# Kernel tuning notes

Hardware: AMD Instinct MI355X
Metric: run time of the kernel (lower is better)

## Reference

```python
import jax, jax.numpy as jnp
import numpy as np
from jax import lax

DIM = 256
STATE = 64
D_INNER = 256          # ssd_expand=1 * dim
HIDDEN = 4 * DIM       # mlp_ratio=4
CONV_DIM = 3 * STATE
B, H, W = 16, 64, 64
EPS = 1e-5


def dwconv(x, w, b=None):
    # depthwise 3x3, SAME padding; x:(B,C,H,W) w:(C,1,3,3)
    y = lax.conv_general_dilated(x, w, (1, 1), 'SAME',
                                 feature_group_count=x.shape[1],
                                 dimension_numbers=('NCHW', 'OIHW', 'NCHW'))
    if b is not None:
        y = y + b[None, :, None, None]
    return y


def batchnorm(x, g, b):
    m = x.mean(axis=(0, 2, 3), keepdims=True)
    v = x.var(axis=(0, 2, 3), keepdims=True)
    return (x - m) * jax.lax.rsqrt(v + EPS) * g[None, :, None, None] + b[None, :, None, None]


def layernorm1d(x, w, b):
    # norm over channel dim of (B,C,L)
    m = x.mean(axis=1, keepdims=True)
    v = x.var(axis=1, keepdims=True)
    return (x - m) * jax.lax.rsqrt(v + EPS) * w[None, :, None] + b[None, :, None]


def pw1d(x, w, b):
    # 1x1 conv1d: x:(B,Cin,L), w:(Cout,Cin)
    return jnp.einsum('oc,bcl->bol', w, x) + b[None, :, None]


def setup_inputs() -> dict:
    key = jax.random.key(0)
    ks = jax.random.split(key, 16)
    s = 0.02
    inp = {
        'x': jax.random.normal(ks[0], (B, DIM, H, W), jnp.float32),
        'alpha': 1e-4 * jnp.ones((4, DIM), jnp.float32),
        'dw1_w': s * jax.random.normal(ks[1], (DIM, 1, 3, 3), jnp.float32),
        'bn1_g': jnp.ones((DIM,), jnp.float32),
        'bn1_b': jnp.zeros((DIM,), jnp.float32),
        'dw2_w': s * jax.random.normal(ks[2], (DIM, 1, 3, 3), jnp.float32),
        'bn2_g': jnp.ones((DIM,), jnp.float32),
        'bn2_b': jnp.zeros((DIM,), jnp.float32),
        'ln_w': jnp.ones((DIM,), jnp.float32),
        'ln_b': jnp.zeros((DIM,), jnp.float32),
        'bcdt_w': s * jax.random.normal(ks[3], (CONV_DIM, DIM), jnp.float32),
        'bcdt_b': jnp.zeros((CONV_DIM,), jnp.float32),
        'mdw_w': s * jax.random.normal(ks[4], (CONV_DIM, 1, 3, 3), jnp.float32),
        'mdw_b': jnp.zeros((CONV_DIM,), jnp.float32),
        'hz_w': s * jax.random.normal(ks[5], (2 * D_INNER, DIM), jnp.float32),
        'hz_b': jnp.zeros((2 * D_INNER,), jnp.float32),
        'out_w': s * jax.random.normal(ks[6], (DIM, D_INNER), jnp.float32),
        'out_b': jnp.zeros((DIM,), jnp.float32),
        'A': jax.random.uniform(ks[7], (STATE,), jnp.float32, 1.0, 16.0),
        'D': jnp.ones((1,), jnp.float32),
        'ffn_w1': s * jax.random.normal(ks[8], (HIDDEN, DIM), jnp.float32),
        'ffn_b1': jnp.zeros((HIDDEN,), jnp.float32),
        'ffn_w2': s * jax.random.normal(ks[9], (DIM, HIDDEN), jnp.float32),
        'ffn_b2': jnp.zeros((DIM,), jnp.float32),
    }
    return inp


def _mixer(xf, bcdt_w, bcdt_b, mdw_w, mdw_b, hz_w, hz_b, out_w, out_b, A, D, h_, w_):
    # xf: (B, dim, L)
    b = xf.shape[0]
    BCdt = pw1d(xf, bcdt_w, bcdt_b).reshape(b, CONV_DIM, h_, w_)
    BCdt = dwconv(BCdt, mdw_w, mdw_b).reshape(b, CONV_DIM, h_ * w_)
    Bm, Cm, dt = jnp.split(BCdt, [STATE, 2 * STATE], axis=1)  # (B,S,L) each
    Am = jax.nn.softmax(dt + A[None, :, None], axis=-1)
    AB = Am * Bm                                   # (B,S,L)
    h = jnp.einsum('bcl,bsl->bcs', xf, AB)         # (B,dim,S) small
    hz = jnp.einsum('oc,bcs->bos', hz_w, h) + hz_b[None, :, None]
    hh, z = jnp.split(hz, [D_INNER], axis=1)
    hh = hh * jax.nn.silu(z) + hh * D[0]
    hh = jnp.einsum('oc,bcs->bos', out_w, hh) + out_b[None, :, None]
    y = jnp.einsum('bcs,bsl->bcl', hh, Cm)         # (B,dim,L)
    return y.reshape(b, DIM, h_, w_)


def reference(x, alpha, dw1_w, bn1_g, bn1_b, dw2_w, bn2_g, bn2_b, ln_w, ln_b,
              bcdt_w, bcdt_b, mdw_w, mdw_b, hz_w, hz_b, out_w, out_b, A, D,
              ffn_w1, ffn_b1, ffn_w2, ffn_b2):
    a = jax.nn.sigmoid(alpha)[:, None, :, None, None]  # (4,1,dim,1,1)
    x = (1 - a[0]) * x + a[0] * batchnorm(dwconv(x, dw1_w), bn1_g, bn1_b)
    x_prev = x
    b, _, h_, w_ = x.shape
    xf = layernorm1d(x.reshape(b, DIM, h_ * w_), ln_w, ln_b)
    y = _mixer(xf, bcdt_w, bcdt_b, mdw_w, mdw_b, hz_w, hz_b, out_w, out_b, A, D, h_, w_)
    x = (1 - a[1]) * x_prev + a[1] * y
    x = (1 - a[2]) * x + a[2] * batchnorm(dwconv(x, dw2_w), bn2_g, bn2_b)
    # FFN: 1x1 conv -> GELU -> 1x1 conv
    hdn = jax.nn.gelu(jnp.einsum('oc,bchw->bohw', ffn_w1, x) + ffn_b1[None, :, None, None])
    x_ffn = jnp.einsum('oc,bchw->bohw', ffn_w2, hdn) + ffn_b2[None, :, None, None]
    x = (1 - a[3]) * x + a[3] * x_ffn
    return x
```

## Files before the change

### kernel.cpp

```cpp
#include <hip/hip_runtime.h>
#include <stdint.h>


typedef __attribute__((ext_vector_type(8))) short bf16x8;
typedef __attribute__((ext_vector_type(4))) float f32x4;

__device__ __forceinline__ unsigned short f2b(float f){
  union { float f; unsigned int u; } v; v.f = f;
  unsigned int r = v.u + 0x7FFFu + ((v.u >> 16) & 1u);
  return (unsigned short)(r >> 16);
}
__device__ __forceinline__ float b2f(unsigned short h){
  union { unsigned int u; float f; } v; v.u = ((unsigned int)h) << 16;
  return v.f;
}
__device__ __forceinline__ float sigm(float x){ return 1.0f / (1.0f + __expf(-x)); }
__device__ __forceinline__ float gelu_fast(float v){
  float t = v * (-2.3022059f - 0.10294886f * v * v);
  float e = __builtin_amdgcn_exp2f(t);
  return v * __builtin_amdgcn_rcpf(1.0f + e);
}
__device__ __forceinline__ unsigned int cvtpk(float lo, float hi){
  unsigned int r;
  asm volatile("v_cvt_pk_bf16_f32 %0, %1, %2" : "=v"(r) : "v"(lo), "v"(hi));
  return r;
}
__device__ __forceinline__ f32x4 mfma16(bf16x8 a, bf16x8 b, f32x4 c){
  return __builtin_amdgcn_mfma_f32_16x16x32_bf16(a, b, c, 0, 0, 0);
}
__device__ __forceinline__ bf16x8 ldb8g(const unsigned short* p){
  return *reinterpret_cast<const bf16x8*>(p);
}
__device__ __forceinline__ f32x4 zero4(){ f32x4 v = {0.f, 0.f, 0.f, 0.f}; return v; }
__device__ __forceinline__ void gload_lds16(const unsigned short* g, unsigned short* l){
  __builtin_amdgcn_global_load_lds(
      (const __attribute__((address_space(1))) void*)g,
      (__attribute__((address_space(3))) void*)l, 16, 0, 0);
}

__global__ __launch_bounds__(256) void k_setup(
    const float* __restrict__ w1, const float* __restrict__ w2,
    const float* __restrict__ bw, const float* __restrict__ hzw,
    const float* __restrict__ outw,
    unsigned short* __restrict__ w1b, unsigned short* __restrict__ w2b,
    unsigned short* __restrict__ bwb, unsigned short* __restrict__ hzwb,
    unsigned short* __restrict__ outwb){
  int tid = blockIdx.x * 256 + threadIdx.x;
  if (tid < 1024 * 256){ w1b[tid] = f2b(w1[tid]); w2b[tid] = f2b(w2[tid]); }
  if (tid < 192 * 256)  bwb[tid] = f2b(bw[tid]);
  if (tid < 512 * 256)  hzwb[tid] = f2b(hzw[tid]);
  if (tid < 256 * 256)  outwb[tid] = f2b(outw[tid]);
}

__global__ __launch_bounds__(256) void k_conv_stats(
    const float* __restrict__ x, const float* __restrict__ w,
    float* __restrict__ bnsum, float* __restrict__ bnsq){
  __shared__ float t[66 * 66];
  __shared__ float rs[4], rq[4];
  int bc = blockIdx.x; int c = bc & 255;
  const float* xp = x + (size_t)bc * 4096;
  int tid = threadIdx.x;
  for (int i = tid; i < 66 * 66; i += 256) t[i] = 0.f;
  __syncthreads();
  #pragma unroll
  for (int j = 0; j < 4; j++){
    int p4 = tid + j * 256;
    float4 v = reinterpret_cast<const float4*>(xp)[p4];
    int p = p4 * 4; int y = p >> 6, xx = p & 63;
    int base = (y + 1) * 66 + xx + 1;
    t[base] = v.x; t[base + 1] = v.y; t[base + 2] = v.z; t[base + 3] = v.w;
  }
  __syncthreads();
  float w0 = w[c*9+0], w1 = w[c*9+1], w2 = w[c*9+2], w3 = w[c*9+3], w4 = w[c*9+4];
  float w5 = w[c*9+5], w6 = w[c*9+6], w7 = w[c*9+7], w8 = w[c*9+8];
  float s = 0.f, q = 0.f;
  #pragma unroll
  for (int j = 0; j < 16; j++){
    int p = tid + j * 256; int y = p >> 6, xx = p & 63;
    const float* r0 = &t[y * 66 + xx];
    float v = r0[0]*w0 + r0[1]*w1 + r0[2]*w2 + r0[66]*w3 + r0[67]*w4 + r0[68]*w5
            + r0[132]*w6 + r0[133]*w7 + r0[134]*w8;
    s += v; q += v * v;
  }
  #pragma unroll
  for (int off = 32; off > 0; off >>= 1){ s += __shfl_down(s, off); q += __shfl_down(q, off); }
  if ((tid & 63) == 0){ rs[tid >> 6] = s; rq[tid >> 6] = q; }
  __syncthreads();
  if (tid == 0){
    atomicAdd(&bnsum[c], rs[0] + rs[1] + rs[2] + rs[3]);
    atomicAdd(&bnsq[c],  rq[0] + rq[1] + rq[2] + rq[3]);
  }
}

__global__ __launch_bounds__(256) void k_conv_bn_blend(
    const float* __restrict__ x, const float* __restrict__ w,
    const float* __restrict__ bnsum, const float* __restrict__ bnsq,
    const float* __restrict__ g, const float* __restrict__ bb,
    const float* __restrict__ alpha, float* __restrict__ out){
  __shared__ float t[66 * 66];
  int bc = blockIdx.x; int c = bc & 255;
  const float* xp = x + (size_t)bc * 4096;
  float* op = out + (size_t)bc * 4096;
  int tid = threadIdx.x;
  for (int i = tid; i < 66 * 66; i += 256) t[i] = 0.f;
  __syncthreads();
  #pragma unroll
  for (int j = 0; j < 4; j++){
    int p4 = tid + j * 256;
    float4 v = reinterpret_cast<const float4*>(xp)[p4];
    int p = p4 * 4; int y = p >> 6, xx = p & 63;
    int base = (y + 1) * 66 + xx + 1;
    t[base] = v.x; t[base + 1] = v.y; t[base + 2] = v.z; t[base + 3] = v.w;
  }
  __syncthreads();
  float w0 = w[c*9+0], w1 = w[c*9+1], w2 = w[c*9+2], w3 = w[c*9+3], w4 = w[c*9+4];
  float w5 = w[c*9+5], w6 = w[c*9+6], w7 = w[c*9+7], w8 = w[c*9+8];
  float m  = bnsum[c] * (1.f / 65536.f);
  float var = bnsq[c] * (1.f / 65536.f) - m * m;
  float sc = rsqrtf(var + 1e-5f) * g[c];
  float bias = bb[c];
  float a = sigm(alpha[c]);
  #pragma unroll
  for (int j = 0; j < 16; j++){
    int p = tid + j * 256; int y = p >> 6, xx = p & 63;
    const float* r0 = &t[y * 66 + xx];
    float v = r0[0]*w0 + r0[1]*w1 + r0[2]*w2 + r0[66]*w3 + r0[67]*w4 + r0[68]*w5
            + r0[132]*w6 + r0[133]*w7 + r0[134]*w8;
    float xv = t[(y + 1) * 66 + xx + 1];
    op[p] = (1.f - a) * xv + a * ((v - m) * sc + bias);
  }
}

__global__ __launch_bounds__(256) void k_ln(
    const float* __restrict__ x1, const float* __restrict__ lnw,
    const float* __restrict__ lnb, unsigned short* __restrict__ xf,
    unsigned short* __restrict__ xfT){
  __shared__ unsigned short st[256 * 65];
  __shared__ float reds[4][64], redq[4][64];
  int b = blockIdx.x >> 6, lt = blockIdx.x & 63; int l0 = lt * 64;
  int t = threadIdx.x, w = t >> 6, lane = t & 63;
  const float* xp = x1 + ((size_t)b * 256) * 4096 + l0 + lane;
  float s = 0.f, q = 0.f;
  for (int i = 0; i < 64; i++){
    int c = w * 64 + i;
    float v = xp[(size_t)c * 4096];
    s += v; q += v * v;
    st[c * 65 + lane] = f2b(v);
  }
  reds[w][lane] = s; redq[w][lane] = q;
  __syncthreads();
  s = reds[0][lane] + reds[1][lane] + reds[2][lane] + reds[3][lane];
  q = redq[0][lane] + redq[1][lane] + redq[2][lane] + redq[3][lane];
  float m = s * (1.f / 256.f);
  float r = rsqrtf(q * (1.f / 256.f) - m * m + 1e-5f);
  for (int i = 0; i < 64; i++){
    int c = w * 64 + i;
    float v = b2f(st[c * 65 + lane]);
    unsigned short h = f2b((v - m) * r * lnw[c] + lnb[c]);
    st[c * 65 + lane] = h;
    xf[((size_t)(b * 256 + c)) * 4096 + l0 + lane] = h;
  }
  __syncthreads();
  int p = t >> 4, cc = t & 15;
  for (int pi = 0; pi < 4; pi++){
    int px = p + pi * 16;
    #pragma unroll
    for (int j = 0; j < 2; j++){
      int c0 = (j * 16 + cc) * 8;
      unsigned short vv[8];
      #pragma unroll
      for (int k = 0; k < 8; k++) vv[k] = st[(c0 + k) * 65 + px];
      *reinterpret_cast<uint4*>(&xfT[((size_t)(b * 4096 + l0 + px)) * 256 + c0]) =
          *reinterpret_cast<uint4*>(vv);
    }
  }
}

__global__ __launch_bounds__(256) void k_xt(
    const float* __restrict__ x, unsigned short* __restrict__ xT){
  __shared__ unsigned short st[256 * 65];
  int b = blockIdx.x >> 6, lt = blockIdx.x & 63; int l0 = lt * 64;
  int t = threadIdx.x, w = t >> 6, lane = t & 63;
  const float* xp = x + ((size_t)b * 256) * 4096 + l0 + lane;
  for (int i = 0; i < 64; i++){
    int c = w * 64 + i;
    st[c * 65 + lane] = f2b(xp[(size_t)c * 4096]);
  }
  __syncthreads();
  int p = t >> 4, cc = t & 15;
  for (int pi = 0; pi < 4; pi++){
    int px = p + pi * 16;
    #pragma unroll
    for (int j = 0; j < 2; j++){
      int c0 = (j * 16 + cc) * 8;
      unsigned short vv[8];
      #pragma unroll
      for (int k = 0; k < 8; k++) vv[k] = st[(c0 + k) * 65 + px];
      *reinterpret_cast<uint4*>(&xT[((size_t)(b * 4096 + l0 + px)) * 256 + c0]) =
          *reinterpret_cast<uint4*>(vv);
    }
  }
}

__global__ __launch_bounds__(256) void k_bcdt(
    const unsigned short* __restrict__ xfT, const unsigned short* __restrict__ wb,
    const float* __restrict__ bias, unsigned short* __restrict__ outp){
  int blk = blockIdx.x; int b = blk >> 6, lt = blk & 63; int l0 = lt * 64;
  int t = threadIdx.x; int wv = t >> 6, lane = t & 63;
  int col = lane & 15, g = lane >> 4;
  f32x4 acc[3][4];
  #pragma unroll
  for (int mm = 0; mm < 3; mm++)
    #pragma unroll
    for (int nn = 0; nn < 4; nn++) acc[mm][nn] = zero4();
  for (int k = 0; k < 8; k++){
    bf16x8 av[3], bv[4];
    #pragma unroll
    for (int mm = 0; mm < 3; mm++){
      int o = (wv * 3 + mm) * 16 + col;
      av[mm] = ldb8g(&wb[(size_t)o * 256 + k * 32 + g * 8]);
    }
    #pragma unroll
    for (int nn = 0; nn < 4; nn++){
      int l = l0 + nn * 16 + col;
      bv[nn] = ldb8g(&xfT[((size_t)(b * 4096 + l)) * 256 + k * 32 + g * 8]);
    }
    #pragma unroll
    for (int mm = 0; mm < 3; mm++)
      #pragma unroll
      for (int nn = 0; nn < 4; nn++) acc[mm][nn] = mfma16(av[mm], bv[nn], acc[mm][nn]);
  }
  #pragma unroll
  for (int mm = 0; mm < 3; mm++)
    #pragma unroll
    for (int nn = 0; nn < 4; nn++)
      #pragma unroll
      for (int r = 0; r < 4; r++){
        int o = (wv * 3 + mm) * 16 + g * 4 + r;
        int l = l0 + nn * 16 + col;
        outp[((size_t)(b * 192 + o)) * 4096 + l] = f2b(acc[mm][nn][r] + bias[o]);
      }
}

__global__ __launch_bounds__(256) void k_conv_mid(
    const unsigned short* __restrict__ in, const float* __restrict__ w,
    const float* __restrict__ wbias, unsigned short* __restrict__ outp,
    float* __restrict__ smmax, float* __restrict__ smsum){
  __shared__ float t[66 * 66];
  __shared__ float red[8];
  int blk = blockIdx.x; int b = blk / 192, ch = blk % 192;
  const unsigned short* xp = in + (size_t)blk * 4096;
  unsigned short* op = outp + (size_t)blk * 4096;
  int tid = threadIdx.x;
  for (int i = tid; i < 66 * 66; i += 256) t[i] = 0.f;
  __syncthreads();
  #pragma unroll
  for (int j = 0; j < 2; j++){
    int p8 = tid + j * 256;
    unsigned short vv[8];
    *reinterpret_cast<uint4*>(vv) = reinterpret_cast<const uint4*>(xp)[p8];
    int p = p8 * 8; int y = p >> 6, xx = p & 63;
    int base = (y + 1) * 66 + xx + 1;
    #pragma unroll
    for (int k = 0; k < 8; k++) t[base + k] = b2f(vv[k]);
  }
  __syncthreads();
  float w0 = w[ch*9+0], w1 = w[ch*9+1], w2 = w[ch*9+2], w3 = w[ch*9+3], w4 = w[ch*9+4];
  float w5 = w[ch*9+5], w6 = w[ch*9+6], w7 = w[ch*9+7], w8 = w[ch*9+8];
  float bv = wbias[ch];
  float vloc[16];
  float mx = -1e30f;
  #pragma unroll
  for (int j = 0; j < 16; j++){
    int p = tid + j * 256; int y = p >> 6, xx = p & 63;
    const float* r0 = &t[y * 66 + xx];
    float v = r0[0]*w0 + r0[1]*w1 + r0[2]*w2 + r0[66]*w3 + r0[67]*w4 + r0[68]*w5
            + r0[132]*w6 + r0[133]*w7 + r0[134]*w8 + bv;
    unsigned short h = f2b(v);
    op[p] = h;
    float vb = b2f(h);
    vloc[j] = vb;
    mx = fmaxf(mx, vb);
  }
  if (ch >= 128){
    #pragma unroll
    for (int off = 32; off > 0; off >>= 1) mx = fmaxf(mx, __shfl_down(mx, off));
    if ((tid & 63) == 0) red[tid >> 6] = mx;
    __syncthreads();
    float M = fmaxf(fmaxf(red[0], red[1]), fmaxf(red[2], red[3]));
    float se = 0.f;
    #pragma unroll
    for (int j = 0; j < 16; j++) se += __expf(vloc[j] - M);
    #pragma unroll
    for (int off = 32; off > 0; off >>= 1) se += __shfl_down(se, off);
    if ((tid & 63) == 0) red[4 + (tid >> 6)] = se;
    __syncthreads();
    if (tid == 0){
      smmax[b * 64 + ch - 128] = M;
      smsum[b * 64 + ch - 128] = red[4] + red[5] + red[6] + red[7];
    }
  }
}

__global__ __launch_bounds__(256) void k_ab(
    const unsigned short* __restrict__ bc, const float* __restrict__ smmax,
    const float* __restrict__ smsum, unsigned short* __restrict__ ab){
  int blk = blockIdx.x; int b = blk >> 6, s = blk & 63;
  const unsigned short* dt = bc + ((size_t)(b * 192 + 128 + s)) * 4096;
  const unsigned short* bm = bc + ((size_t)(b * 192 + s)) * 4096;
  unsigned short* o = ab + ((size_t)(b * 64 + s)) * 4096;
  float M = smmax[b * 64 + s];
  float inv = 1.f / smsum[b * 64 + s];
  for (int i = threadIdx.x; i < 4096; i += 256)
    o[i] = f2b(__expf(b2f(dt[i]) - M) * inv * b2f(bm[i]));
}

__global__ __launch_bounds__(256) void k_cmt(
    const unsigned short* __restrict__ bc, unsigned short* __restrict__ cmt){
  __shared__ float t[64 * 65];
  int blk = blockIdx.x; int b = blk >> 6, lt = blk & 63; int l0 = lt * 64;
  int tid = threadIdx.x;
  #pragma unroll
  for (int it = 0; it < 2; it++){
    int row = (tid >> 3) + it * 32;
    int lq = (tid & 7) * 8;
    const unsigned short* p = bc + ((size_t)(b * 192 + 64 + row)) * 4096 + l0 + lq;
    unsigned short vv[8];
    *reinterpret_cast<uint4*>(vv) = *reinterpret_cast<const uint4*>(p);
    #pragma unroll
    for (int k = 0; k < 8; k++) t[row * 65 + lq + k] = b2f(vv[k]);
  }
  __syncthreads();
  #pragma unroll
  for (int it = 0; it < 2; it++){
    int l = (tid >> 3) + it * 32;
    int sq = (tid & 7) * 8;
    unsigned short vv[8];
    #pragma unroll
    for (int k = 0; k < 8; k++) vv[k] = f2b(t[(sq + k) * 65 + l]);
    *reinterpret_cast<uint4*>(&cmt[((size_t)(b * 4096 + l0 + l)) * 64 + sq]) =
        *reinterpret_cast<uint4*>(vv);
  }
}

__global__ __launch_bounds__(512) void k_h(
    const unsigned short* __restrict__ ab, const unsigned short* __restrict__ xf,
    float* __restrict__ hpart){
  int blk = blockIdx.x; int b = blk & 15, chunk = blk >> 4;
  int t = threadIdx.x; int wv = t >> 6, lane = t & 63;
  int col = lane & 15, g = lane >> 4;
  int mt = wv & 3, nh = wv >> 2;
  f32x4 acc[8];
  #pragma unroll
  for (int nn = 0; nn < 8; nn++) acc[nn] = zero4();
  int lbase = chunk * 256;
  const unsigned short* ap = ab + ((size_t)(b * 64 + mt * 16 + col)) * 4096 + lbase + g * 8;
  for (int ks = 0; ks < 8; ks++){
    bf16x8 av = ldb8g(ap + ks * 32);
    #pragma unroll
    for (int nn = 0; nn < 8; nn++){
      int c = nh * 128 + nn * 16 + col;
      bf16x8 bv = ldb8g(&xf[((size_t)(b * 256 + c)) * 4096 + lbase + ks * 32 + g * 8]);
      acc[nn] = mfma16(av, bv, acc[nn]);
    }
  }
  #pragma unroll
  for (int nn = 0; nn < 8; nn++)
    #pragma unroll
    for (int r = 0; r < 4; r++){
      int s = mt * 16 + g * 4 + r;
      int c = nh * 128 + nn * 16 + col;
      hpart[(((size_t)chunk * 16 + b) * 64 + s) * 256 + c] = acc[nn][r];
    }
}

__global__ __launch_bounds__(256) void k_hsum(
    const float* __restrict__ hp, unsigned short* __restrict__ hsb){
  int i = blockIdx.x * 256 + threadIdx.x;
  float s = 0.f;
  #pragma unroll
  for (int c = 0; c < 16; c++) s += hp[(size_t)c * 262144 + i];
  hsb[i] = f2b(s);
}

__global__ __launch_bounds__(256) void k_hz(
    const unsigned short* __restrict__ hsb, const unsigned short* __restrict__ hzwb,
    const float* __restrict__ hzb, const float* __restrict__ Dp,
    unsigned short* __restrict__ hh1b){
  int blk = blockIdx.x; int b = blk >> 2, og = blk & 3;
  int t = threadIdx.x, wv = t >> 6, lane = t & 63;
  int col = lane & 15, g = lane >> 4;
  int ou = og * 64 + wv * 16;
  int oz = 256 + ou;
  f32x4 au[4], az[4];
  #pragma unroll
  for (int nn = 0; nn < 4; nn++){ au[nn] = zero4(); az[nn] = zero4(); }
  const unsigned short* bbase = hsb + (size_t)b * 64 * 256;
  for (int k = 0; k < 8; k++){
    bf16x8 a_u = ldb8g(&hzwb[(size_t)(ou + col) * 256 + k * 32 + g * 8]);
    bf16x8 a_z = ldb8g(&hzwb[(size_t)(oz + col) * 256 + k * 32 + g * 8]);
    bf16x8 bv[4];
    #pragma unroll
    for (int nn = 0; nn < 4; nn++)
      bv[nn] = ldb8g(bbase + (size_t)(nn * 16 + col) * 256 + k * 32 + g * 8);
    #pragma unroll
    for (int nn = 0; nn < 4; nn++){
      au[nn] = mfma16(a_u, bv[nn], au[nn]);
      az[nn] = mfma16(a_z, bv[nn], az[nn]);
    }
  }
  float Dv = Dp[0];
  #pragma unroll
  for (int nn = 0; nn < 4; nn++){
    int s = nn * 16 + col;
    float hv[4];
    #pragma unroll
    for (int r = 0; r < 4; r++){
      int o = ou + g * 4 + r;
      float u = au[nn][r] + hzb[o];
      float z = az[nn][r] + hzb[o + 256];
      float sl = z / (1.f + __expf(-z));
      hv[r] = u * (sl + Dv);
    }
    unsigned int p0 = cvtpk(hv[0], hv[1]), p1 = cvtpk(hv[2], hv[3]);
    uint2 pv; pv.x = p0; pv.y = p1;
    *reinterpret_cast<uint2*>(&hh1b[((size_t)(b * 64 + s)) * 256 + ou + g * 4]) = pv;
  }
}

__global__ __launch_bounds__(256) void k_out(
    const unsigned short* __restrict__ hh1b, const unsigned short* __restrict__ outwb,
    const float* __restrict__ ob, unsigned short* __restrict__ hh2){
  int blk = blockIdx.x; int b = blk >> 2, dg = blk & 3;
  int t = threadIdx.x, wv = t >> 6, lane = t & 63;
  int col = lane & 15, g = lane >> 4;
  int d0 = dg * 64 + wv * 16;
  f32x4 acc[4];
  #pragma unroll
  for (int nn = 0; nn < 4; nn++) acc[nn] = zero4();
  const unsigned short* bbase = hh1b + (size_t)b * 64 * 256;
  for (int k = 0; k < 8; k++){
    bf16x8 a = ldb8g(&outwb[(size_t)(d0 + col) * 256 + k * 32 + g * 8]);
    bf16x8 bv[4];
    #pragma unroll
    for (int nn = 0; nn < 4; nn++)
      bv[nn] = ldb8g(bbase + (size_t)(nn * 16 + col) * 256 + k * 32 + g * 8);
    #pragma unroll
    for (int nn = 0; nn < 4; nn++) acc[nn] = mfma16(a, bv[nn], acc[nn]);
  }
  #pragma unroll
  for (int nn = 0; nn < 4; nn++){
    int s = nn * 16 + col;
    #pragma unroll
    for (int r = 0; r < 4; r++){
      int d = d0 + g * 4 + r;
      hh2[((size_t)(b * 256 + d)) * 64 + s] = f2b(acc[nn][r] + ob[d]);
    }
  }
}

__global__ __launch_bounds__(256) void k_y_blend(
    const unsigned short* __restrict__ hh2, const unsigned short* __restrict__ cmt,
    const float* __restrict__ alpha, float* __restrict__ x){
  int blk = blockIdx.x; int b = blk >> 6, lt = blk & 63; int l0 = lt * 64;
  int t = threadIdx.x; int wv = t >> 6, lane = t & 63;
  int col = lane & 15, g = lane >> 4;
  f32x4 acc[4][4];
  #pragma unroll
  for (int mm = 0; mm < 4; mm++)
    #pragma unroll
    for (int nn = 0; nn < 4; nn++) acc[mm][nn] = zero4();
  #pragma unroll
  for (int k = 0; k < 2; k++){
    bf16x8 av[4], bv[4];
    #pragma unroll
    for (int mm = 0; mm < 4; mm++){
      int c = (wv * 4 + mm) * 16 + col;
      av[mm] = ldb8g(&hh2[((size_t)(b * 256 + c)) * 64 + k * 32 + g * 8]);
    }
    #pragma unroll
    for (int nn = 0; nn < 4; nn++){
      int l = l0 + nn * 16 + col;
      bv[nn] = ldb8g(&cmt[((size_t)(b * 4096 + l)) * 64 + k * 32 + g * 8]);
    }
    #pragma unroll
    for (int mm = 0; mm < 4; mm++)
      #pragma unroll
      for (int nn = 0; nn < 4; nn++) acc[mm][nn] = mfma16(av[mm], bv[nn], acc[mm][nn]);
  }
  #pragma unroll
  for (int mm = 0; mm < 4; mm++)
    #pragma unroll
    for (int r = 0; r < 4; r++){
      int c = (wv * 4 + mm) * 16 + g * 4 + r;
      float a1 = sigm(alpha[c]);
      #pragma unroll
      for (int nn = 0; nn < 4; nn++){
        int l = l0 + nn * 16 + col;
        size_t idx = ((size_t)(b * 256 + c)) * 4096 + l;
        float xv = x[idx];
        x[idx] = (1.f - a1) * xv + a1 * acc[mm][nn][r];
      }
    }
}

__global__ __launch_bounds__(256, 4) void k_ffn1(
    const unsigned short* __restrict__ xT, const unsigned short* __restrict__ w1b,
    const float* __restrict__ b1, unsigned short* __restrict__ Hh, int b0){
  __shared__ unsigned short smem[17408];
  unsigned short* At = smem;
  unsigned short* Bt = smem + 8192;
  int wk = ((blockIdx.x & 7) << 8) + (blockIdx.x >> 3);
  int mt = wk & 7, nt = wk >> 3;
  int t = threadIdx.x, wv = t >> 6, lane = t & 63;
  int col = lane & 15, g = lane >> 4;
  int wr = wv >> 1, wc = wv & 1;
  const unsigned short* ag = w1b + (size_t)(mt * 128) * 256;
  const unsigned short* bg = xT + ((size_t)b0 * 4096 + (size_t)nt * 128) * 256;
  f32x4 acc[4][4];
  #pragma unroll
  for (int mm = 0; mm < 4; mm++)
    #pragma unroll
    for (int nn = 0; nn < 4; nn++) acc[mm][nn] = zero4();
  for (int kk = 0; kk < 4; kk++){
    __syncthreads();
    #pragma unroll
    for (int j = 0; j < 4; j++){
      int id = t + j * 256;
      int row = id >> 3, kc = (id & 7) * 8;
      gload_lds16(ag + (size_t)row * 256 + kk * 64 + kc, At + id * 8);
      gload_lds16(bg + (size_t)row * 256 + kk * 64 + kc, Bt + id * 8);
    }
    __syncthreads();
    #pragma unroll
    for (int ks = 0; ks < 2; ks++){
      bf16x8 av[4], bv[4];
      #pragma unroll
      for (int mm = 0; mm < 4; mm++)
        av[mm] = *reinterpret_cast<const bf16x8*>(&At[(wr * 64 + mm * 16 + col) * 64 + ks * 32 + g * 8]);
      #pragma unroll
      for (int nn = 0; nn < 4; nn++)
        bv[nn] = *reinterpret_cast<const bf16x8*>(&Bt[(wc * 64 + nn * 16 + col) * 64 + ks * 32 + g * 8]);
      #pragma unroll
      for (int mm = 0; mm < 4; mm++)
        #pragma unroll
        for (int nn = 0; nn < 4; nn++)
          acc[mm][nn] = mfma16(av[mm], bv[nn], acc[mm][nn]);
    }
  }
  __syncthreads();
  #pragma unroll
  for (int mm = 0; mm < 4; mm++){
    int o4 = wr * 64 + mm * 16 + g * 4;
    #pragma unroll
    for (int nn = 0; nn < 4; nn++){
      int lloc = wc * 64 + nn * 16 + col;
      float gv[4];
      #pragma unroll
      for (int r = 0; r < 4; r++)
        gv[r] = gelu_fast(acc[mm][nn][r] + b1[mt * 128 + o4 + r]);
      uint2 pv; pv.x = cvtpk(gv[0], gv[1]); pv.y = cvtpk(gv[2], gv[3]);
      *reinterpret_cast<uint2*>(&smem[lloc * 136 + o4]) = pv;
    }
  }
  __syncthreads();
  size_t hb = (size_t)nt * 128;
  #pragma unroll
  for (int j = 0; j < 8; j++){
    int id = t + j * 256;
    int l = id >> 4, oc = id & 15;
    uint4 v = *reinterpret_cast<const uint4*>(&smem[l * 136 + oc * 8]);
    *reinterpret_cast<uint4*>(&Hh[(hb + l) * 1024 + mt * 128 + oc * 8]) = v;
  }
}

__global__ __launch_bounds__(256, 4) void k_ffn2(
    const unsigned short* __restrict__ Hh, const unsigned short* __restrict__ w2b,
    const float* __restrict__ b2, const float* __restrict__ alpha3,
    float* __restrict__ x, int b0){
  __shared__ unsigned short smem[16384];
  unsigned short* At = smem;
  unsigned short* Bt = smem + 8192;
  int wk = ((blockIdx.x & 7) << 6) + (blockIdx.x >> 3);
  int mt = wk & 1, nt = wk >> 1;
  int t = threadIdx.x, wv = t >> 6, lane = t & 63;
  int col = lane & 15, g = lane >> 4;
  int wr = wv >> 1, wc = wv & 1;
  const unsigned short* ag = w2b + (size_t)(mt * 128) * 1024;
  const unsigned short* bg = Hh + (size_t)(nt * 128) * 1024;
  f32x4 acc[4][4];
  #pragma unroll
  for (int mm = 0; mm < 4; mm++)
    #pragma unroll
    for (int nn = 0; nn < 4; nn++) acc[mm][nn] = zero4();
  for (int kk = 0; kk < 16; kk++){
    __syncthreads();
    #pragma unroll
    for (int j = 0; j < 4; j++){
      int id = t + j * 256;
      int row = id >> 3, kc = (id & 7) * 8;
      gload_lds16(ag + (size_t)row * 1024 + kk * 64 + kc, At + id * 8);
      gload_lds16(bg + (size_t)row * 1024 + kk * 64 + kc, Bt + id * 8);
    }
    __syncthreads();
    #pragma unroll
    for (int ks = 0; ks < 2; ks++){
      bf16x8 av[4], bv[4];
      #pragma unroll
      for (int mm = 0; mm < 4; mm++)
        av[mm] = *reinterpret_cast<const bf16x8*>(&At[(wr * 64 + mm * 16 + col) * 64 + ks * 32 + g * 8]);
      #pragma unroll
      for (int nn = 0; nn < 4; nn++)
        bv[nn] = *reinterpret_cast<const bf16x8*>(&Bt[(wc * 64 + nn * 16 + col) * 64 + ks * 32 + g * 8]);
      #pragma unroll
      for (int mm = 0; mm < 4; mm++)
        #pragma unroll
        for (int nn = 0; nn < 4; nn++)
          acc[mm][nn] = mfma16(av[mm], bv[nn], acc[mm][nn]);
    }
  }
  #pragma unroll
  for (int mm = 0; mm < 4; mm++)
    #pragma unroll
    for (int r = 0; r < 4; r++){
      int d = mt * 128 + wr * 64 + mm * 16 + g * 4 + r;
      float a3 = sigm(alpha3[d]);
      float bias = b2[d];
      #pragma unroll
      for (int nn = 0; nn < 4; nn++){
        int lh = nt * 128 + wc * 64 + nn * 16 + col;
        int b = b0 + (lh >> 12);
        int l = lh & 4095;
        size_t idx = ((size_t)(b * 256 + d)) * 4096 + l;
        float xv = x[idx];
        x[idx] = (1.f - a3) * xv + a3 * (acc[mm][nn][r] + bias);
      }
    }
}

extern "C" void kernel_launch(void* const* d_in, const int* in_sizes, int n_in,
                              void* d_out, int out_size, void* d_ws, size_t ws_size,
                              hipStream_t stream){
  (void)in_sizes; (void)n_in; (void)out_size; (void)ws_size;
  const float* x      = (const float*)d_in[0];
  const float* alpha  = (const float*)d_in[1];
  const float* dw1_w  = (const float*)d_in[2];
  const float* bn1_g  = (const float*)d_in[3];
  const float* bn1_b  = (const float*)d_in[4];
  const float* dw2_w  = (const float*)d_in[5];
  const float* bn2_g  = (const float*)d_in[6];
  const float* bn2_b  = (const float*)d_in[7];
  const float* ln_w   = (const float*)d_in[8];
  const float* ln_b   = (const float*)d_in[9];
  const float* bcdt_w = (const float*)d_in[10];
  const float* bcdt_b = (const float*)d_in[11];
  const float* mdw_w  = (const float*)d_in[12];
  const float* mdw_b  = (const float*)d_in[13];
  const float* hz_w   = (const float*)d_in[14];
  const float* hz_b   = (const float*)d_in[15];
  const float* out_w  = (const float*)d_in[16];
  const float* out_b  = (const float*)d_in[17];
  const float* Dvec   = (const float*)d_in[19];
  const float* ffn_w1 = (const float*)d_in[20];
  const float* ffn_b1 = (const float*)d_in[21];
  const float* ffn_w2 = (const float*)d_in[22];
  const float* ffn_b2 = (const float*)d_in[23];
  float* out = (float*)d_out;
  char* ws = (char*)d_ws;

  const size_t OFF_BCRAW = 0;
  const size_t OFF_BCC   = 25165824;
  const size_t OFF_XF    = 50331648;
  const size_t OFF_XFT   = 83886080;
  const size_t OFF_AB    = 0;
  const size_t OFF_CMT   = 8388608;
  const size_t OFF_HPART = 16777216;
  const size_t OFF_HSB   = 83886080;
  const size_t OFF_HH1B  = 84410368;
  const size_t OFF_HH2   = 84934656;
  const size_t OFF_H     = 0;
  const size_t OFF_X3T   = 67108864;
  const size_t OFF_W1B   = 117440512;
  const size_t OFF_W2B   = 117964800;
  const size_t OFF_BWB   = 118489088;
  const size_t OFF_HZWB  = 118587392;
  const size_t OFF_OUTWB = 119111680;
  const size_t OFF_STATS = 119373824;
  const size_t OFF_SMMAX = 119377920;
  const size_t OFF_SMSUM = 119382016;

  unsigned short* bcraw = (unsigned short*)(ws + OFF_BCRAW);
  unsigned short* bcc   = (unsigned short*)(ws + OFF_BCC);
  unsigned short* xf    = (unsigned short*)(ws + OFF_XF);
  unsigned short* xfT   = (unsigned short*)(ws + OFF_XFT);
  unsigned short* ab    = (unsigned short*)(ws + OFF_AB);
  unsigned short* cmt   = (unsigned short*)(ws + OFF_CMT);
  float* hpart = (float*)(ws + OFF_HPART);
  unsigned short* hsb  = (unsigned short*)(ws + OFF_HSB);
  unsigned short* hh1b = (unsigned short*)(ws + OFF_HH1B);
  unsigned short* hh2  = (unsigned short*)(ws + OFF_HH2);
  unsigned short* Hbuf = (unsigned short*)(ws + OFF_H);
  unsigned short* x3T  = (unsigned short*)(ws + OFF_X3T);
  unsigned short* w1b = (unsigned short*)(ws + OFF_W1B);
  unsigned short* w2b = (unsigned short*)(ws + OFF_W2B);
  unsigned short* bwb = (unsigned short*)(ws + OFF_BWB);
  unsigned short* hzwb  = (unsigned short*)(ws + OFF_HZWB);
  unsigned short* outwb = (unsigned short*)(ws + OFF_OUTWB);
  float* bn1sum = (float*)(ws + OFF_STATS);
  float* bn1sq  = bn1sum + 256;
  float* bn2sum = bn1sum + 512;
  float* bn2sq  = bn1sum + 768;
  float* smmax = (float*)(ws + OFF_SMMAX);
  float* smsum = (float*)(ws + OFF_SMSUM);

  hipMemsetAsync(ws + OFF_STATS, 0, 4096, stream);
  k_setup<<<1024, 256, 0, stream>>>(ffn_w1, ffn_w2, bcdt_w, hz_w, out_w,
                                    w1b, w2b, bwb, hzwb, outwb);
  k_conv_stats<<<4096, 256, 0, stream>>>(x, dw1_w, bn1sum, bn1sq);
  k_conv_bn_blend<<<4096, 256, 0, stream>>>(x, dw1_w, bn1sum, bn1sq,
                                            bn1_g, bn1_b, alpha + 0, out);
  k_ln<<<1024, 256, 0, stream>>>(out, ln_w, ln_b, xf, xfT);
  k_bcdt<<<1024, 256, 0, stream>>>(xfT, bwb, bcdt_b, bcraw);
  k_conv_mid<<<3072, 256, 0, stream>>>(bcraw, mdw_w, mdw_b, bcc, smmax, smsum);
  k_ab<<<1024, 256, 0, stream>>>(bcc, smmax, smsum, ab);
  k_cmt<<<1024, 256, 0, stream>>>(bcc, cmt);
  k_h<<<256, 512, 0, stream>>>(ab, xf, hpart);
  k_hsum<<<1024, 256, 0, stream>>>(hpart, hsb);
  k_hz<<<64, 256, 0, stream>>>(hsb, hzwb, hz_b, Dvec, hh1b);
  k_out<<<64, 256, 0, stream>>>(hh1b, outwb, out_b, hh2);
  k_y_blend<<<1024, 256, 0, stream>>>(hh2, cmt, alpha + 256, out);
  k_conv_stats<<<4096, 256, 0, stream>>>(out, dw2_w, bn2sum, bn2sq);
  k_conv_bn_blend<<<4096, 256, 0, stream>>>(out, dw2_w, bn2sum, bn2sq,
                                            bn2_g, bn2_b, alpha + 512, out);
  k_xt<<<1024, 256, 0, stream>>>(out, x3T);
  k_ffn1<<<2048, 256, 0, stream>>>(x3T, w1b, ffn_b1, Hbuf, 0);
  k_ffn2<<<512, 256, 0, stream>>>(Hbuf, w2b, ffn_b2, alpha + 768, out, 0);
  k_ffn1<<<2048, 256, 0, stream>>>(x3T, w1b, ffn_b1, Hbuf, 8);
  k_ffn2<<<512, 256, 0, stream>>>(Hbuf, w2b, ffn_b2, alpha + 768, out, 8);
}
```

Before: 387.2 us.

## Fuse softmax-B into h GEMM, merge hsum/hz/out kernels, swizzle ffn1 LDS

Computes the softmax-weighted B operand inside k_h from bcc and the softmax statistics, which removes the k_ab kernel and its intermediate buffer. Partial h results are now stored in bf16, and one k_hzout kernel per batch reduces them, runs the hz GEMM with SiLU gating and then the out projection, keeping the intermediates in LDS. This replaces the separate k_hsum, k_hz and k_out kernels. k_ffn1 gets an XOR-swizzled unpadded LDS tile, hoisted bias loads and launch bounds raised to 5; the fused k_hzout launches only 16 blocks and the bf16 partials lose precision.

```diff
diff --git a/kernel.cpp b/kernel.cpp
--- a/kernel.cpp
+++ b/kernel.cpp
@@ -302,19 +302,6 @@
   }
 }
 
-__global__ __launch_bounds__(256) void k_ab(
-    const unsigned short* __restrict__ bc, const float* __restrict__ smmax,
-    const float* __restrict__ smsum, unsigned short* __restrict__ ab){
-  int blk = blockIdx.x; int b = blk >> 6, s = blk & 63;
-  const unsigned short* dt = bc + ((size_t)(b * 192 + 128 + s)) * 4096;
-  const unsigned short* bm = bc + ((size_t)(b * 192 + s)) * 4096;
-  unsigned short* o = ab + ((size_t)(b * 64 + s)) * 4096;
-  float M = smmax[b * 64 + s];
-  float inv = 1.f / smsum[b * 64 + s];
-  for (int i = threadIdx.x; i < 4096; i += 256)
-    o[i] = f2b(__expf(b2f(dt[i]) - M) * inv * b2f(bm[i]));
-}
-
 __global__ __launch_bounds__(256) void k_cmt(
     const unsigned short* __restrict__ bc, unsigned short* __restrict__ cmt){
   __shared__ float t[64 * 65];
@@ -344,19 +331,34 @@
 }
 
 __global__ __launch_bounds__(512) void k_h(
-    const unsigned short* __restrict__ ab, const unsigned short* __restrict__ xf,
-    float* __restrict__ hpart){
+    const unsigned short* __restrict__ bcc, const float* __restrict__ smmax,
+    const float* __restrict__ smsum, const unsigned short* __restrict__ xf,
+    unsigned short* __restrict__ hpart){
   int blk = blockIdx.x; int b = blk & 15, chunk = blk >> 4;
   int t = threadIdx.x; int wv = t >> 6, lane = t & 63;
   int col = lane & 15, g = lane >> 4;
   int mt = wv & 3, nh = wv >> 2;
+  int sA = mt * 16 + col;
+  float M = smmax[b * 64 + sA];
+  float inv = 1.f / smsum[b * 64 + sA];
   f32x4 acc[8];
   #pragma unroll
   for (int nn = 0; nn < 8; nn++) acc[nn] = zero4();
   int lbase = chunk * 256;
-  const unsigned short* ap = ab + ((size_t)(b * 64 + mt * 16 + col)) * 4096 + lbase + g * 8;
+  const unsigned short* dtp = bcc + ((size_t)(b * 192 + 128 + sA)) * 4096 + lbase + g * 8;
+  const unsigned short* bmp = bcc + ((size_t)(b * 192 + sA)) * 4096 + lbase + g * 8;
   for (int ks = 0; ks < 8; ks++){
-    bf16x8 av = ldb8g(ap + ks * 32);
+    unsigned short d8[8], m8[8];
+    *reinterpret_cast<uint4*>(d8) = *reinterpret_cast<const uint4*>(dtp + ks * 32);
+    *reinterpret_cast<uint4*>(m8) = *reinterpret_cast<const uint4*>(bmp + ks * 32);
+    unsigned int pk[4];
+    #pragma unroll
+    for (int j = 0; j < 4; j++){
+      float v0 = __expf(b2f(d8[2*j])   - M) * inv * b2f(m8[2*j]);
+      float v1 = __expf(b2f(d8[2*j+1]) - M) * inv * b2f(m8[2*j+1]);
+      pk[j] = cvtpk(v0, v1);
+    }
+    bf16x8 av = *reinterpret_cast<bf16x8*>(pk);
     #pragma unroll
     for (int nn = 0; nn < 8; nn++){
       int c = nh * 128 + nn * 16 + col;
@@ -370,91 +372,107 @@
     for (int r = 0; r < 4; r++){
       int s = mt * 16 + g * 4 + r;
       int c = nh * 128 + nn * 16 + col;
-      hpart[(((size_t)chunk * 16 + b) * 64 + s) * 256 + c] = acc[nn][r];
-    }
-}
-
-__global__ __launch_bounds__(256) void k_hsum(
-    const float* __restrict__ hp, unsigned short* __restrict__ hsb){
-  int i = blockIdx.x * 256 + threadIdx.x;
-  float s = 0.f;
-  #pragma unroll
-  for (int c = 0; c < 16; c++) s += hp[(size_t)c * 262144 + i];
-  hsb[i] = f2b(s);
-}
-
-__global__ __launch_bounds__(256) void k_hz(
-    const unsigned short* __restrict__ hsb, const unsigned short* __restrict__ hzwb,
+      hpart[(((size_t)chunk * 16 + b) * 64 + s) * 256 + c] = f2b(acc[nn][r]);
+    }
+}
+
+__global__ __launch_bounds__(512) void k_hzout(
+    const unsigned short* __restrict__ hpart, const unsigned short* __restrict__ hzwb,
     const float* __restrict__ hzb, const float* __restrict__ Dp,
-    unsigned short* __restrict__ hh1b){
-  int blk = blockIdx.x; int b = blk >> 2, og = blk & 3;
+    const unsigned short* __restrict__ outwb, const float* __restrict__ ob,
+    unsigned short* __restrict__ hh2){
+  __shared__ unsigned short hs[64 * 264];
+  __shared__ unsigned short h1[64 * 264];
+  int b = blockIdx.x;
   int t = threadIdx.x, wv = t >> 6, lane = t & 63;
   int col = lane & 15, g = lane >> 4;
-  int ou = og * 64 + wv * 16;
-  int oz = 256 + ou;
-  f32x4 au[4], az[4];
-  #pragma unroll
-  for (int nn = 0; nn < 4; nn++){ au[nn] = zero4(); az[nn] = zero4(); }
-  const unsigned short* bbase = hsb + (size_t)b * 64 * 256;
-  for (int k = 0; k < 8; k++){
-    bf16x8 a_u = ldb8g(&hzwb[(size_t)(ou + col) * 256 + k * 32 + g * 8]);
-    bf16x8 a_z = ldb8g(&hzwb[(size_t)(oz + col) * 256 + k * 32 + g * 8]);
-    bf16x8 bv[4];
-    #pragma unroll
-    for (int nn = 0; nn < 4; nn++)
-      bv[nn] = ldb8g(bbase + (size_t)(nn * 16 + col) * 256 + k * 32 + g * 8);
+  {
+    int i0 = t * 32;
+    int srow = i0 >> 8, c0 = i0 & 255;
+    float acc[32];
+    #pragma unroll
+    for (int j = 0; j < 32; j++) acc[j] = 0.f;
+    for (int ch = 0; ch < 16; ch++){
+      const unsigned short* p = hpart + ((size_t)(ch * 16 + b)) * 16384 + i0;
+      #pragma unroll
+      for (int q = 0; q < 4; q++){
+        unsigned short v8[8];
+        *reinterpret_cast<uint4*>(v8) = *reinterpret_cast<const uint4*>(p + q * 8);
+        #pragma unroll
+        for (int k = 0; k < 8; k++) acc[q * 8 + k] += b2f(v8[k]);
+      }
+    }
+    #pragma unroll
+    for (int q = 0; q < 4; q++){
+      unsigned int pk[4];
+      #pragma unroll
+      for (int j = 0; j < 4; j++) pk[j] = cvtpk(acc[q*8 + 2*j], acc[q*8 + 2*j + 1]);
+      *reinterpret_cast<uint4*>(&hs[srow * 264 + c0 + q * 8]) =
+          *reinterpret_cast<uint4*>(pk);
+    }
+  }
+  __syncthreads();
+  float Dv = Dp[0];
+  #pragma unroll
+  for (int ss = 0; ss < 2; ss++){
+    int ou = wv * 32 + ss * 16;
+    int oz = 256 + ou;
+    f32x4 au[4], az[4];
+    #pragma unroll
+    for (int nn = 0; nn < 4; nn++){ au[nn] = zero4(); az[nn] = zero4(); }
+    for (int k = 0; k < 8; k++){
+      bf16x8 a_u = ldb8g(&hzwb[(size_t)(ou + col) * 256 + k * 32 + g * 8]);
+      bf16x8 a_z = ldb8g(&hzwb[(size_t)(oz + col) * 256 + k * 32 + g * 8]);
+      bf16x8 bv[4];
+      #pragma unroll
+      for (int nn = 0; nn < 4; nn++)
+        bv[nn] = *reinterpret_cast<const bf16x8*>(&hs[(nn * 16 + col) * 264 + k * 32 + g * 8]);
+      #pragma unroll
+      for (int nn = 0; nn < 4; nn++){
+        au[nn] = mfma16(a_u, bv[nn], au[nn]);
+        az[nn] = mfma16(a_z, bv[nn], az[nn]);
+      }
+    }
     #pragma unroll
     for (int nn = 0; nn < 4; nn++){
-      au[nn] = mfma16(a_u, bv[nn], au[nn]);
-      az[nn] = mfma16(a_z, bv[nn], az[nn]);
-    }
-  }
-  float Dv = Dp[0];
-  #pragma unroll
-  for (int nn = 0; nn < 4; nn++){
-    int s = nn * 16 + col;
-    float hv[4];
-    #pragma unroll
-    for (int r = 0; r < 4; r++){
-      int o = ou + g * 4 + r;
-      float u = au[nn][r] + hzb[o];
-      float z = az[nn][r] + hzb[o + 256];
-      float sl = z / (1.f + __expf(-z));
-      hv[r] = u * (sl + Dv);
-    }
-    unsigned int p0 = cvtpk(hv[0], hv[1]), p1 = cvtpk(hv[2], hv[3]);
-    uint2 pv; pv.x = p0; pv.y = p1;
-    *reinterpret_cast<uint2*>(&hh1b[((size_t)(b * 64 + s)) * 256 + ou + g * 4]) = pv;
-  }
-}
-
-__global__ __launch_bounds__(256) void k_out(
-    const unsigned short* __restrict__ hh1b, const unsigned short* __restrict__ outwb,
-    const float* __restrict__ ob, unsigned short* __restrict__ hh2){
-  int blk = blockIdx.x; int b = blk >> 2, dg = blk & 3;
-  int t = threadIdx.x, wv = t >> 6, lane = t & 63;
-  int col = lane & 15, g = lane >> 4;
-  int d0 = dg * 64 + wv * 16;
-  f32x4 acc[4];
-  #pragma unroll
-  for (int nn = 0; nn < 4; nn++) acc[nn] = zero4();
-  const unsigned short* bbase = hh1b + (size_t)b * 64 * 256;
-  for (int k = 0; k < 8; k++){
-    bf16x8 a = ldb8g(&outwb[(size_t)(d0 + col) * 256 + k * 32 + g * 8]);
-    bf16x8 bv[4];
-    #pragma unroll
-    for (int nn = 0; nn < 4; nn++)
-      bv[nn] = ldb8g(bbase + (size_t)(nn * 16 + col) * 256 + k * 32 + g * 8);
-    #pragma unroll
-    for (int nn = 0; nn < 4; nn++) acc[nn] = mfma16(a, bv[nn], acc[nn]);
-  }
-  #pragma unroll
-  for (int nn = 0; nn < 4; nn++){
-    int s = nn * 16 + col;
-    #pragma unroll
-    for (int r = 0; r < 4; r++){
-      int d = d0 + g * 4 + r;
-      hh2[((size_t)(b * 256 + d)) * 64 + s] = f2b(acc[nn][r] + ob[d]);
+      int s = nn * 16 + col;
+      float hv[4];
+      #pragma unroll
+      for (int r = 0; r < 4; r++){
+        int o = ou + g * 4 + r;
+        float u = au[nn][r] + hzb[o];
+        float z = az[nn][r] + hzb[o + 256];
+        float sl = z / (1.f + __expf(-z));
+        hv[r] = u * (sl + Dv);
+      }
+      uint2 pv; pv.x = cvtpk(hv[0], hv[1]); pv.y = cvtpk(hv[2], hv[3]);
+      *reinterpret_cast<uint2*>(&h1[s * 264 + ou + g * 4]) = pv;
+    }
+  }
+  __syncthreads();
+  #pragma unroll
+  for (int ss = 0; ss < 2; ss++){
+    int d0 = wv * 32 + ss * 16;
+    f32x4 acc[4];
+    #pragma unroll
+    for (int nn = 0; nn < 4; nn++) acc[nn] = zero4();
+    for (int k = 0; k < 8; k++){
+      bf16x8 a = ldb8g(&outwb[(size_t)(d0 + col) * 256 + k * 32 + g * 8]);
+      bf16x8 bv[4];
+      #pragma unroll
+      for (int nn = 0; nn < 4; nn++)
+        bv[nn] = *reinterpret_cast<const bf16x8*>(&h1[(nn * 16 + col) * 264 + k * 32 + g * 8]);
+      #pragma unroll
+      for (int nn = 0; nn < 4; nn++) acc[nn] = mfma16(a, bv[nn], acc[nn]);
+    }
+    #pragma unroll
+    for (int nn = 0; nn < 4; nn++){
+      int s = nn * 16 + col;
+      #pragma unroll
+      for (int r = 0; r < 4; r++){
+        int d = d0 + g * 4 + r;
+        hh2[((size_t)(b * 256 + d)) * 64 + s] = f2b(acc[nn][r] + ob[d]);
+      }
     }
   }
 }
@@ -504,10 +522,10 @@
     }
 }
 
-__global__ __launch_bounds__(256, 4) void k_ffn1(
+__global__ __launch_bounds__(256, 5) void k_ffn1(
     const unsigned short* __restrict__ xT, const unsigned short* __restrict__ w1b,
     const float* __restrict__ b1, unsigned short* __restrict__ Hh, int b0){
-  __shared__ unsigned short smem[17408];
+  __shared__ unsigned short smem[16384];
   unsigned short* At = smem;
   unsigned short* Bt = smem + 8192;
   int wk = ((blockIdx.x & 7) << 8) + (blockIdx.x >> 3);
@@ -517,6 +535,12 @@
   int wr = wv >> 1, wc = wv & 1;
   const unsigned short* ag = w1b + (size_t)(mt * 128) * 256;
   const unsigned short* bg = xT + ((size_t)b0 * 4096 + (size_t)nt * 128) * 256;
+  float bias[4][4];
+  #pragma unroll
+  for (int mm = 0; mm < 4; mm++)
+    #pragma unroll
+    for (int r = 0; r < 4; r++)
+      bias[mm][r] = b1[mt * 128 + wr * 64 + mm * 16 + g * 4 + r];
   f32x4 acc[4][4];
   #pragma unroll
   for (int mm = 0; mm < 4; mm++)
@@ -549,6 +573,7 @@
     }
   }
   __syncthreads();
+  char* sm8 = (char*)smem;
   #pragma unroll
   for (int mm = 0; mm < 4; mm++){
     int o4 = wr * 64 + mm * 16 + g * 4;
@@ -558,9 +583,10 @@
       float gv[4];
       #pragma unroll
       for (int r = 0; r < 4; r++)
-        gv[r] = gelu_fast(acc[mm][nn][r] + b1[mt * 128 + o4 + r]);
+        gv[r] = gelu_fast(acc[mm][nn][r] + bias[mm][r]);
       uint2 pv; pv.x = cvtpk(gv[0], gv[1]); pv.y = cvtpk(gv[2], gv[3]);
-      *reinterpret_cast<uint2*>(&smem[lloc * 136 + o4]) = pv;
+      int byte = (lloc * 256 + o4 * 2) ^ ((lloc & 7) << 4);
+      *reinterpret_cast<uint2*>(sm8 + byte) = pv;
     }
   }
   __syncthreads();
@@ -569,12 +595,13 @@
   for (int j = 0; j < 8; j++){
     int id = t + j * 256;
     int l = id >> 4, oc = id & 15;
-    uint4 v = *reinterpret_cast<const uint4*>(&smem[l * 136 + oc * 8]);
+    int byte = (l * 256 + oc * 16) ^ ((l & 7) << 4);
+    uint4 v = *reinterpret_cast<const uint4*>(sm8 + byte);
     *reinterpret_cast<uint4*>(&Hh[(hb + l) * 1024 + mt * 128 + oc * 8]) = v;
   }
 }
 
-__global__ __launch_bounds__(256, 4) void k_ffn2(
+__global__ __launch_bounds__(256, 5) void k_ffn2(
     const unsigned short* __restrict__ Hh, const unsigned short* __restrict__ w2b,
     const float* __restrict__ b2, const float* __restrict__ alpha3,
     float* __restrict__ x, int b0){
@@ -672,11 +699,8 @@
   const size_t OFF_BCC   = 25165824;
   const size_t OFF_XF    = 50331648;
   const size_t OFF_XFT   = 83886080;
-  const size_t OFF_AB    = 0;
   const size_t OFF_CMT   = 8388608;
   const size_t OFF_HPART = 16777216;
-  const size_t OFF_HSB   = 83886080;
-  const size_t OFF_HH1B  = 84410368;
   const size_t OFF_HH2   = 84934656;
   const size_t OFF_H     = 0;
   const size_t OFF_X3T   = 67108864;
@@ -693,14 +717,11 @@
   unsigned short* bcc   = (unsigned short*)(ws + OFF_BCC);
   unsigned short* xf    = (unsigned short*)(ws + OFF_XF);
   unsigned short* xfT   = (unsigned short*)(ws + OFF_XFT);
-  unsigned short* ab    = (unsigned short*)(ws + OFF_AB);
   unsigned short* cmt   = (unsigned short*)(ws + OFF_CMT);
-  float* hpart = (float*)(ws + OFF_HPART);
-  unsigned short* hsb  = (unsigned short*)(ws + OFF_HSB);
-  unsigned short* hh1b = (unsigned short*)(ws + OFF_HH1B);
-  unsigned short* hh2  = (unsigned short*)(ws + OFF_HH2);
-  unsigned short* Hbuf = (unsigned short*)(ws + OFF_H);
-  unsigned short* x3T  = (unsigned short*)(ws + OFF_X3T);
+  unsigned short* hpart = (unsigned short*)(ws + OFF_HPART);
+  unsigned short* hh2   = (unsigned short*)(ws + OFF_HH2);
+  unsigned short* Hbuf  = (unsigned short*)(ws + OFF_H);
+  unsigned short* x3T   = (unsigned short*)(ws + OFF_X3T);
   unsigned short* w1b = (unsigned short*)(ws + OFF_W1B);
   unsigned short* w2b = (unsigned short*)(ws + OFF_W2B);
   unsigned short* bwb = (unsigned short*)(ws + OFF_BWB);
@@ -722,12 +743,9 @@
   k_ln<<<1024, 256, 0, stream>>>(out, ln_w, ln_b, xf, xfT);
   k_bcdt<<<1024, 256, 0, stream>>>(xfT, bwb, bcdt_b, bcraw);
   k_conv_mid<<<3072, 256, 0, stream>>>(bcraw, mdw_w, mdw_b, bcc, smmax, smsum);
-  k_ab<<<1024, 256, 0, stream>>>(bcc, smmax, smsum, ab);
   k_cmt<<<1024, 256, 0, stream>>>(bcc, cmt);
-  k_h<<<256, 512, 0, stream>>>(ab, xf, hpart);
-  k_hsum<<<1024, 256, 0, stream>>>(hpart, hsb);
-  k_hz<<<64, 256, 0, stream>>>(hsb, hzwb, hz_b, Dvec, hh1b);
-  k_out<<<64, 256, 0, stream>>>(hh1b, outwb, out_b, hh2);
+  k_h<<<256, 512, 0, stream>>>(bcc, smmax, smsum, xf, hpart);
+  k_hzout<<<16, 512, 0, stream>>>(hpart, hzwb, hz_b, Dvec, outwb, out_b, hh2);
   k_y_blend<<<1024, 256, 0, stream>>>(hh2, cmt, alpha + 256, out);
   k_conv_stats<<<4096, 256, 0, stream>>>(out, dw2_w, bn2sum, bn2sq);
   k_conv_bn_blend<<<4096, 256, 0, stream>>>(out, dw2_w, bn2sum, bn2sq,
```

Measured after the change: 604.2 us. +56.0%, slower.
